# Kernel tuning notes

Hardware: AMD Instinct MI355X
Metric: run time of the kernel (lower is better)

The kernel has to match this reference:

```python
import jax, jax.numpy as jnp
import numpy as np

B, C_MEL, D_RES, TX, TY = 16, 80, 256, 1024, 4096
NEG = -1e9


def seq_mask(lengths, max_len):
    return (jnp.arange(max_len)[None, :] < lengths[:, None]).astype(jnp.float32)


def maximum_path(value, mask):
    # value, mask: [b, tx, ty]. Glow-TTS style monotonic-alignment Viterbi DP.
    b, t_x, t_y = value.shape
    value = value * mask
    x_range = jnp.arange(t_x)[None, :]  # [1, tx]

    def fwd_step(v, inp):
        val_j, j = inp  # val_j: [b, tx]
        v_prev = jnp.pad(v, ((0, 0), (1, 0)), constant_values=NEG)[:, :-1]  # v[x-1]
        stay = v >= v_prev  # True -> best path stays at same x
        v_max = jnp.where(stay, v, v_prev)
        v_new = jnp.where(x_range <= j, v_max + val_j, NEG)
        return v_new, stay

    _, stays = jax.lax.scan(
        fwd_step,
        jnp.zeros((b, t_x), value.dtype),
        (jnp.moveaxis(value, 2, 0), jnp.arange(t_y)),
    )  # stays: [ty, b, tx] bool
    mask_t = jnp.moveaxis(mask, 2, 0)  # [ty, b, tx]
    dirs = jnp.where(mask_t > 0, stays.astype(jnp.int32), 1)  # outside mask: stay

    idx0 = jnp.sum(mask[:, :, 0], axis=1).astype(jnp.int32) - 1  # x_length - 1
    barange = jnp.arange(b)

    def bwd_step(idx, dir_j):  # dir_j: [b, tx]
        row = jax.nn.one_hot(idx, t_x, dtype=value.dtype)  # [b, tx]
        idx_new = idx + dir_j[barange, idx] - 1
        return idx_new, row

    _, path = jax.lax.scan(bwd_step, idx0, dirs, reverse=True)  # [ty, b, tx]
    return jnp.transpose(path, (1, 2, 0)) * mask  # [b, tx, ty]


def setup_inputs() -> dict:
    key = jax.random.key(0)
    k1, k2, k3, k4, k5, k6 = jax.random.split(key, 6)
    return {
        "x_m": jax.random.normal(k1, (B, C_MEL, TX), jnp.float32),
        "x_res": jax.random.normal(k2, (B, D_RES, TX), jnp.float32),
        "mel": jax.random.normal(k3, (B, C_MEL, TY), jnp.float32),
        "x_lengths": jax.random.randint(k4, (B,), TX // 2, TX + 1, jnp.int32),
        "mel_lengths": jax.random.randint(k5, (B,), TY // 2, TY + 1, jnp.int32),
        "noise": jax.random.normal(k6, (B, C_MEL, TY), jnp.float32),
    }


def reference(x_m, x_res, mel, x_lengths, mel_lengths, noise):
    x_mask = seq_mask(x_lengths, TX)[:, None, :]   # [b, 1, tx]
    z_mask = seq_mask(mel_lengths, TY)[:, None, :]  # [b, 1, ty]
    attn_mask = x_mask[:, 0, :, None] * z_mask[:, 0, None, :]  # [b, tx, ty]

    # correlation-style score: -||x_m||^2 - ||mel||^2 + 2 x_m^T mel
    x2 = -jnp.sum(x_m ** 2, axis=1)[:, :, None]   # [b, tx, 1]
    z2 = -jnp.sum(mel ** 2, axis=1)[:, None, :]   # [b, 1, ty]
    xz2 = jnp.einsum("bct,bcs->bts", x_m, mel)    # [b, tx, ty]
    corr = x2 + z2 + 2.0 * xz2

    attn = maximum_path(corr, attn_mask)  # [b, tx, ty], no_grad in original

    z_m = jnp.einsum("bts,bct->bcs", attn, x_res)       # [b, d_res, ty]
    mel_proj = jnp.einsum("bts,bct->bcs", attn, x_m) + noise  # [b, n_mels, ty]
    mel_proj_loss = jnp.mean(jnp.abs((mel_proj - mel) * z_mask))
    logw_ = jnp.log(1e-8 + jnp.sum(attn, axis=-1))[:, None, :] * x_mask  # [b, 1, tx]
    return z_m, z_mask, attn, logw_, mel_proj_loss, mel_proj
```

## Files before the change

### kernel.cpp

```cpp
#include <hip/hip_runtime.h>
#include <cstdint>
#include <cstddef>

typedef unsigned int u32;
typedef unsigned short u16;

#define BB 16
#define CMEL 80
#define DRES 256
#define TXN 1024
#define TYN 4096
#define NEGV (-1e9f)

#define OFF_ZM    0ull
#define OFF_ZMASK 16777216ull
#define OFF_ATTN  16842752ull
#define OFF_LOGW  83951616ull
#define OFF_LOSS  83968000ull
#define OFF_MPROJ 83968001ull

#define WS_X2   0
#define WS_Z2   262144
#define WS_IDX  1310720
#define WS_PART 1572864

__global__ __launch_bounds__(1024) void k1_prep(
    const float* __restrict__ xm, const float* __restrict__ mel,
    const int* __restrict__ mlen,
    float* __restrict__ x2n, float* __restrict__ z2n, float* __restrict__ out_zmask) {
  int b = blockIdx.x;
  int slice = blockIdx.y;
  int t = threadIdx.x;
  if (slice == 0) {
    float acc = 0.f;
    const float* p = xm + (size_t)b * CMEL * TXN + t;
    #pragma unroll 4
    for (int c = 0; c < CMEL; ++c) { float v = p[(size_t)c * TXN]; acc = fmaf(v, v, acc); }
    x2n[b * TXN + t] = -acc;
  } else {
    int j = (slice - 1) * 1024 + t;
    float acc = 0.f;
    const float* p = mel + (size_t)b * CMEL * TYN + j;
    #pragma unroll 4
    for (int c = 0; c < CMEL; ++c) { float v = p[(size_t)c * TYN]; acc = fmaf(v, v, acc); }
    z2n[b * TYN + j] = -acc;
    out_zmask[b * TYN + j] = (j < mlen[b]) ? 1.0f : 0.0f;
  }
}

__global__ __launch_bounds__(256) void k2_corr(
    const float* __restrict__ xm, const float* __restrict__ mel,
    const float* __restrict__ x2n, const float* __restrict__ z2n,
    const int* __restrict__ xlen, const int* __restrict__ mlen,
    float* __restrict__ valT) {
  int b = blockIdx.z;
  int ml = mlen[b];
  int j0 = blockIdx.y * 128;
  if (j0 >= ml) return;
  int xl = xlen[b];
  int x0 = blockIdx.x * 128;

  __shared__ float sA[40][128];
  __shared__ float sB[40][128];

  int t = threadIdx.x;
  int i16 = t & 15, j16 = t >> 4;

  float acc[2][4][2][4];
  #pragma unroll
  for (int p = 0; p < 2; ++p)
    #pragma unroll
    for (int jj = 0; jj < 4; ++jj)
      #pragma unroll
      for (int q = 0; q < 2; ++q)
        #pragma unroll
        for (int i = 0; i < 4; ++i) acc[p][jj][q][i] = 0.f;

  for (int c0 = 0; c0 < CMEL; c0 += 40) {
    __syncthreads();
    for (int i = t; i < 40 * 32; i += 256) {
      int c = i >> 5, q = i & 31;
      *(float4*)&sA[c][q * 4] =
          *(const float4*)(xm + (size_t)(b * CMEL + c0 + c) * TXN + x0 + q * 4);
      *(float4*)&sB[c][q * 4] =
          *(const float4*)(mel + (size_t)(b * CMEL + c0 + c) * TYN + j0 + q * 4);
    }
    __syncthreads();
    #pragma unroll 2
    for (int c = 0; c < 40; ++c) {
      float av[2][4], bw[2][4];
      *(float4*)av[0] = *(const float4*)&sA[c][i16 * 4];
      *(float4*)av[1] = *(const float4*)&sA[c][64 + i16 * 4];
      *(float4*)bw[0] = *(const float4*)&sB[c][j16 * 4];
      *(float4*)bw[1] = *(const float4*)&sB[c][64 + j16 * 4];
      #pragma unroll
      for (int p = 0; p < 2; ++p)
        #pragma unroll
        for (int jj = 0; jj < 4; ++jj)
          #pragma unroll
          for (int q = 0; q < 2; ++q)
            #pragma unroll
            for (int i = 0; i < 4; ++i)
              acc[p][jj][q][i] = fmaf(av[q][i], bw[p][jj], acc[p][jj][q][i]);
    }
  }

  float4 xa[2];
  xa[0] = *(const float4*)(x2n + b * TXN + x0 + i16 * 4);
  xa[1] = *(const float4*)(x2n + b * TXN + x0 + 64 + i16 * 4);
  int xb0 = x0 + i16 * 4;
  int xb1 = x0 + 64 + i16 * 4;

  #pragma unroll
  for (int p = 0; p < 2; ++p)
    #pragma unroll
    for (int jj = 0; jj < 4; ++jj) {
      int j = j0 + p * 64 + j16 * 4 + jj;
      if (j >= ml) continue;
      float zz = z2n[b * TYN + j];
      float* row = valT + ((size_t)b * TYN + j) * TXN;
      float4 o;
      o.x = (xb0 + 0 < xl) ? ((xa[0].x + zz) + 2.f * acc[p][jj][0][0]) : 0.f;
      o.y = (xb0 + 1 < xl) ? ((xa[0].y + zz) + 2.f * acc[p][jj][0][1]) : 0.f;
      o.z = (xb0 + 2 < xl) ? ((xa[0].z + zz) + 2.f * acc[p][jj][0][2]) : 0.f;
      o.w = (xb0 + 3 < xl) ? ((xa[0].w + zz) + 2.f * acc[p][jj][0][3]) : 0.f;
      *(float4*)(row + xb0) = o;
      o.x = (xb1 + 0 < xl) ? ((xa[1].x + zz) + 2.f * acc[p][jj][1][0]) : 0.f;
      o.y = (xb1 + 1 < xl) ? ((xa[1].y + zz) + 2.f * acc[p][jj][1][1]) : 0.f;
      o.z = (xb1 + 2 < xl) ? ((xa[1].z + zz) + 2.f * acc[p][jj][1][2]) : 0.f;
      o.w = (xb1 + 3 < xl) ? ((xa[1].w + zz) + 2.f * acc[p][jj][1][3]) : 0.f;
      *(float4*)(row + xb1) = o;
    }
}

__global__ __launch_bounds__(64) void k3_dp(
    const float* __restrict__ valT, const int* __restrict__ mlen,
    u32* __restrict__ staysW) {
  int b = blockIdx.x;
  int ml = mlen[b];
  int lane = threadIdx.x;
  int xbase = lane << 4;

  float v[16];
  #pragma unroll
  for (int i = 0; i < 16; ++i) v[i] = NEGV;
  if (lane == 0) v[0] = 0.f;

  float4 pf[8][4];
  #pragma unroll
  for (int k = 0; k < 8; ++k) {
    const float* rowp = valT + (((size_t)(b * TYN + k)) << 10);
    #pragma unroll
    for (int q = 0; q < 4; ++q)
      pf[k][q] = *(const float4*)(rowp + (xbase + (q << 2)));
  }

  u32* swb = staysW + (((size_t)(b * TXN + xbase)) << 7);
  int jpad = (ml + 31) & ~31;

  for (int j0 = 0; j0 < jpad; j0 += 32) {
    u32 bits[16];
    #pragma unroll
    for (int i = 0; i < 16; ++i) bits[i] = 0;

    #pragma unroll
    for (int jj = 0; jj < 32; ++jj) {
      const int j = j0 + jj;
      float e = __shfl_up(v[15], 1);
      if (lane == 0) e = NEGV;

      float val[16];
      #pragma unroll
      for (int q = 0; q < 4; ++q) {
        val[4 * q + 0] = pf[jj & 7][q].x;
        val[4 * q + 1] = pf[jj & 7][q].y;
        val[4 * q + 2] = pf[jj & 7][q].z;
        val[4 * q + 3] = pf[jj & 7][q].w;
      }

      #pragma unroll
      for (int i = 15; i >= 1; --i) {
        bool s = v[i] >= v[i - 1];
        float m = s ? v[i] : v[i - 1];
        v[i] = m + val[i];
        bits[i] |= ((u32)s) << jj;
      }
      {
        bool s = v[0] >= e;
        float m = s ? v[0] : e;
        v[0] = m + val[0];
        bits[0] |= ((u32)s) << jj;
      }

      {
        int lt = (j + 1) >> 4;
        if (lane == lt) v[(jj + 1) & 15] = NEGV;
      }

      {
        int jn = j + 8; if (jn > TYN - 1) jn = TYN - 1;
        const float* rowp = valT + (((size_t)(b * TYN + jn)) << 10);
        #pragma unroll
        for (int q = 0; q < 4; ++q)
          pf[jj & 7][q] = *(const float4*)(rowp + (xbase + (q << 2)));
      }
    }

    const int w = j0 >> 5;
    #pragma unroll
    for (int i = 0; i < 16; ++i) swb[(i << 7) + w] = bits[i];
  }
}

__global__ __launch_bounds__(256) void k4_backtrack(
    const u32* __restrict__ staysW, const int* __restrict__ xlen, const int* __restrict__ mlen,
    int* __restrict__ idxArr, float* __restrict__ out_logw) {
  int b = blockIdx.x;
  int xl = xlen[b], ml = mlen[b];
  int t = threadIdx.x;
  __shared__ u32 win[64][128];
  __shared__ u16 lidx[TYN];
  __shared__ u16 ldur[TXN];
  __shared__ int st[3];

  for (int i = t; i < TXN; i += 256) ldur[i] = 0;
  if (t == 0) { st[0] = xl - 1; st[1] = ml - 1; st[2] = ml - 1; }
  __syncthreads();

  int wb = (xl - 1) >> 6;
  for (int i = t; i < 64 * 128; i += 256) {
    int r = i >> 7, wq = i & 127;
    win[r][wq] = staysW[((size_t)(b * TXN + (wb << 6) + r) << 7) + wq];
  }
  __syncthreads();

  while (true) {
    if (t == 0) {
      int idx = st[0], j = st[1], end = st[2];
      while (j >= 0 && (idx >> 6) == wb) {
        u32 w = win[idx & 63][j >> 5];
        int p = j & 31;
        u32 below = w << (31 - p);
        u32 inv = ~below;
        int ones = (inv != 0u) ? __builtin_clz(inv) : 32;
        if (ones > p) {
          j -= p + 1;
        } else {
          int jz = j - ones;
          for (int q = jz; q <= end; ++q) lidx[q] = (u16)idx;
          ldur[idx] = (u16)(end - jz + 1);
          end = jz - 1;
          j = jz - 1;
          idx -= 1;
        }
      }
      if (j < 0) {
        for (int q = 0; q <= end; ++q) lidx[q] = (u16)idx;
        if (idx >= 0 && end >= 0) ldur[idx] = (u16)(end + 1);
      }
      st[0] = idx; st[1] = j; st[2] = end;
    }
    __syncthreads();
    if (st[1] < 0) break;
    wb = st[0] >> 6;
    for (int i = t; i < 64 * 128; i += 256) {
      int r = i >> 7, wq = i & 127;
      win[r][wq] = staysW[((size_t)(b * TXN + (wb << 6) + r) << 7) + wq];
    }
    __syncthreads();
  }

  for (int q = t; q < TYN; q += 256) idxArr[b * TYN + q] = (q < ml) ? (int)lidx[q] : -1;
  for (int x = t; x < TXN; x += 256)
    out_logw[b * TXN + x] = (x < xl) ? logf(1e-8f + (float)ldur[x]) : 0.f;
}

__global__ __launch_bounds__(256) void k5_attn(
    const int* __restrict__ idxArr, float* __restrict__ attn) {
  int b = blockIdx.z;
  int x = blockIdx.y;
  int j = blockIdx.x * 1024 + threadIdx.x * 4;
  int4 iv = *(const int4*)(idxArr + b * TYN + j);
  float4 o;
  o.x = (iv.x == x) ? 1.f : 0.f;
  o.y = (iv.y == x) ? 1.f : 0.f;
  o.z = (iv.z == x) ? 1.f : 0.f;
  o.w = (iv.w == x) ? 1.f : 0.f;
  *(float4*)(attn + ((size_t)(b * TXN + x)) * TYN + j) = o;
}

__global__ __launch_bounds__(256) void k5_zm(
    const int* __restrict__ idxArr, const float* __restrict__ xres, float* __restrict__ zm) {
  int bid = blockIdx.x; int b = bid >> 8; int c = bid & 255;
  const float* row = xres + (size_t)(b * DRES + c) * TXN;
  float* orow = zm + (size_t)(b * DRES + c) * TYN;
  const int* ia = idxArr + b * TYN;
  for (int j = threadIdx.x; j < TYN; j += 256) {
    int idx = ia[j];
    orow[j] = (idx >= 0) ? row[idx] : 0.f;
  }
}

__global__ __launch_bounds__(256) void k5_mproj(
    const int* __restrict__ idxArr, const float* __restrict__ xm,
    const float* __restrict__ noise, const float* __restrict__ mel,
    float* __restrict__ mproj, float* __restrict__ partials) {
  int bid = blockIdx.x; int b = bid / CMEL; int c = bid % CMEL;
  const float* row  = xm    + (size_t)(b * CMEL + c) * TXN;
  const float* nrow = noise + (size_t)(b * CMEL + c) * TYN;
  const float* mrow = mel   + (size_t)(b * CMEL + c) * TYN;
  float* orow = mproj + (size_t)(b * CMEL + c) * TYN;
  const int* ia = idxArr + b * TYN;
  float acc = 0.f;
  for (int j = threadIdx.x; j < TYN; j += 256) {
    int idx = ia[j];
    float g = (idx >= 0) ? row[idx] : 0.f;
    float mp = g + nrow[j];
    orow[j] = mp;
    float d = mp - mrow[j];
    acc += (idx >= 0) ? fabsf(d) : 0.f;
  }
  #pragma unroll
  for (int o = 32; o; o >>= 1) acc += __shfl_down(acc, o);
  __shared__ float ws4[4];
  if ((threadIdx.x & 63) == 0) ws4[threadIdx.x >> 6] = acc;
  __syncthreads();
  if (threadIdx.x == 0) partials[bid] = (ws4[0] + ws4[1]) + (ws4[2] + ws4[3]);
}

__global__ __launch_bounds__(256) void k6_loss(
    const float* __restrict__ partials, float* __restrict__ out_loss) {
  float acc = 0.f;
  for (int i = threadIdx.x; i < BB * CMEL; i += 256) acc += partials[i];
  #pragma unroll
  for (int o = 32; o; o >>= 1) acc += __shfl_down(acc, o);
  __shared__ float ws4[4];
  if ((threadIdx.x & 63) == 0) ws4[threadIdx.x >> 6] = acc;
  __syncthreads();
  if (threadIdx.x == 0)
    out_loss[0] = ((ws4[0] + ws4[1]) + (ws4[2] + ws4[3])) * (1.0f / ((float)BB * CMEL * TYN));
}

extern "C" void kernel_launch(void* const* d_in, const int* in_sizes, int n_in,
                              void* d_out, int out_size, void* d_ws, size_t ws_size,
                              hipStream_t stream) {
  const float* xm    = (const float*)d_in[0];
  const float* xres  = (const float*)d_in[1];
  const float* mel   = (const float*)d_in[2];
  const int*   xlen  = (const int*)d_in[3];
  const int*   mlen  = (const int*)d_in[4];
  const float* noise = (const float*)d_in[5];

  float* out = (float*)d_out;
  float* out_zm    = out + OFF_ZM;
  float* out_zmask = out + OFF_ZMASK;
  float* out_attn  = out + OFF_ATTN;
  float* out_logw  = out + OFF_LOGW;
  float* out_loss  = out + OFF_LOSS;
  float* out_mproj = out + OFF_MPROJ;

  char* ws = (char*)d_ws;
  float* x2n      = (float*)(ws + WS_X2);
  float* z2n      = (float*)(ws + WS_Z2);
  int*   idxArr   = (int*)(ws + WS_IDX);
  float* partials = (float*)(ws + WS_PART);

  float* valT   = out_attn;
  u32*   staysW = (u32*)out_zm;

  hipLaunchKernelGGL(k1_prep, dim3(BB, 5), dim3(1024), 0, stream, xm, mel, mlen, x2n, z2n, out_zmask);
  hipLaunchKernelGGL(k2_corr, dim3(8, 32, BB), dim3(256), 0, stream, xm, mel, x2n, z2n, xlen, mlen, valT);
  hipLaunchKernelGGL(k3_dp, dim3(BB), dim3(64), 0, stream, valT, mlen, staysW);
  hipLaunchKernelGGL(k4_backtrack, dim3(BB), dim3(256), 0, stream, staysW, xlen, mlen, idxArr, out_logw);
  hipLaunchKernelGGL(k5_attn, dim3(4, TXN, BB), dim3(256), 0, stream, idxArr, out_attn);
  hipLaunchKernelGGL(k5_zm, dim3(BB * DRES), dim3(256), 0, stream, idxArr, xres, out_zm);
  hipLaunchKernelGGL(k5_mproj, dim3(BB * CMEL), dim3(256), 0, stream, idxArr, xm, noise, mel, out_mproj, partials);
  hipLaunchKernelGGL(k6_loss, dim3(1), dim3(256), 0, stream, partials, out_loss);
}
```

Measured before the change: 1.202 ms.

## Stream DP value rows through LDS ring buffer with async global-to-LDS loads

The serial Viterbi DP kernel now prefetches value rows with global_load_lds into a 12-row LDS ring buffer, replacing the 8-deep register prefetch. A manual vmcnt wait keeps about 11 rows in flight, and a small register double-buffer reads from LDS two steps ahead. The bit-packing of stay flags changes from 32-bit words per 32 steps to 16-bit halves per 16 steps, which pads the tail less, and the select is replaced by fmaxf. The aim is to hide global memory latency on the single-wave latency-bound recurrence, at the cost of hand-tuned waitcnt counts and a different stays word layout that the backtrack must still read correctly.

```diff
diff --git a/kernel.cpp b/kernel.cpp
--- a/kernel.cpp
+++ b/kernel.cpp
@@ -23,6 +23,10 @@
 #define WS_Z2   262144
 #define WS_IDX  1310720
 #define WS_PART 1572864
+
+#define GLLDS(gp, lp) \
+  __builtin_amdgcn_global_load_lds((const __attribute__((address_space(1))) void*)(gp), \
+                                   (__attribute__((address_space(3))) void*)(lp), 16, 0, 0)
 
 __global__ __launch_bounds__(1024) void k1_prep(
     const float* __restrict__ xm, const float* __restrict__ mel,
@@ -133,82 +137,107 @@
     }
 }
 
+#define NR 12
 __global__ __launch_bounds__(64) void k3_dp(
     const float* __restrict__ valT, const int* __restrict__ mlen,
     u32* __restrict__ staysW) {
-  int b = blockIdx.x;
-  int ml = mlen[b];
-  int lane = threadIdx.x;
-  int xbase = lane << 4;
+  __shared__ float lds[NR * 1024];
+  const int b = blockIdx.x;
+  const int ml = mlen[b];
+  const int lane = threadIdx.x;
+  const float* vb = valT + ((size_t)b << 22);
+
+  for (int r = 0; r < NR - 1; ++r) {
+    const float* gp = vb + ((size_t)r << 10) + (lane << 4);
+    float* lp = &lds[r << 10];
+    GLLDS(gp,      lp);
+    GLLDS(gp + 4,  lp + 256);
+    GLLDS(gp + 8,  lp + 512);
+    GLLDS(gp + 12, lp + 768);
+  }
 
   float v[16];
   #pragma unroll
   for (int i = 0; i < 16; ++i) v[i] = NEGV;
   if (lane == 0) v[0] = 0.f;
 
-  float4 pf[8][4];
-  #pragma unroll
-  for (int k = 0; k < 8; ++k) {
-    const float* rowp = valT + (((size_t)(b * TYN + k)) << 10);
+  asm volatile("s_waitcnt vmcnt(36)" ::: "memory");
+  float4 vbuf[4][4];
+  #pragma unroll
+  for (int q = 0; q < 4; ++q) {
+    vbuf[0][q] = *(const float4*)&lds[(0 << 10) + (q << 8) + (lane << 2)];
+    vbuf[1][q] = *(const float4*)&lds[(1 << 10) + (q << 8) + (lane << 2)];
+  }
+
+  int wSlot = NR - 1;
+  int rSlot = 2;
+  int gRow  = NR - 1;
+
+  u16* sw16 = (u16*)staysW + (((size_t)(b * TXN + (lane << 4))) << 8);
+
+  const int jpad = (ml + 15) & ~15;
+  for (int j0 = 0; j0 < jpad; j0 += 16) {
+    u32 bh[16];
     #pragma unroll
-    for (int q = 0; q < 4; ++q)
-      pf[k][q] = *(const float4*)(rowp + (xbase + (q << 2)));
-  }
-
-  u32* swb = staysW + (((size_t)(b * TXN + xbase)) << 7);
-  int jpad = (ml + 31) & ~31;
-
-  for (int j0 = 0; j0 < jpad; j0 += 32) {
-    u32 bits[16];
+    for (int i = 0; i < 16; ++i) bh[i] = 0;
+
     #pragma unroll
-    for (int i = 0; i < 16; ++i) bits[i] = 0;
-
+    for (int jj = 0; jj < 16; ++jj) {
+      const int j = j0 + jj;
+
+      {
+        const float* gp = vb + ((size_t)gRow << 10) + (lane << 4);
+        float* lp = &lds[wSlot << 10];
+        GLLDS(gp,      lp);
+        GLLDS(gp + 4,  lp + 256);
+        GLLDS(gp + 8,  lp + 512);
+        GLLDS(gp + 12, lp + 768);
+        wSlot = (wSlot == NR - 1) ? 0 : wSlot + 1;
+        gRow += (gRow < TYN - 1) ? 1 : 0;
+      }
+
+      asm volatile("s_waitcnt vmcnt(36)" ::: "memory");
+
+      {
+        float e = __shfl_up(v[15], 1);
+        if (lane == 0) e = NEGV;
+
+        float val[16];
+        #pragma unroll
+        for (int q = 0; q < 4; ++q) {
+          val[4 * q + 0] = vbuf[jj & 3][q].x;
+          val[4 * q + 1] = vbuf[jj & 3][q].y;
+          val[4 * q + 2] = vbuf[jj & 3][q].z;
+          val[4 * q + 3] = vbuf[jj & 3][q].w;
+        }
+
+        #pragma unroll
+        for (int i = 15; i >= 1; --i) {
+          bool s = v[i] >= v[i - 1];
+          v[i] = fmaxf(v[i], v[i - 1]) + val[i];
+          bh[i] |= ((u32)s) << jj;
+        }
+        {
+          bool s = v[0] >= e;
+          v[0] = fmaxf(v[0], e) + val[0];
+          bh[0] |= ((u32)s) << jj;
+        }
+
+        {
+          int lt = (j + 1) >> 4;
+          if (lane == lt) v[(jj + 1) & 15] = NEGV;
+        }
+      }
+
+      #pragma unroll
+      for (int q = 0; q < 4; ++q)
+        vbuf[(jj + 2) & 3][q] = *(const float4*)&lds[(rSlot << 10) + (q << 8) + (lane << 2)];
+      rSlot = (rSlot == NR - 1) ? 0 : rSlot + 1;
+    }
+
+    const int h = j0 >> 4;
     #pragma unroll
-    for (int jj = 0; jj < 32; ++jj) {
-      const int j = j0 + jj;
-      float e = __shfl_up(v[15], 1);
-      if (lane == 0) e = NEGV;
-
-      float val[16];
-      #pragma unroll
-      for (int q = 0; q < 4; ++q) {
-        val[4 * q + 0] = pf[jj & 7][q].x;
-        val[4 * q + 1] = pf[jj & 7][q].y;
-        val[4 * q + 2] = pf[jj & 7][q].z;
-        val[4 * q + 3] = pf[jj & 7][q].w;
-      }
-
-      #pragma unroll
-      for (int i = 15; i >= 1; --i) {
-        bool s = v[i] >= v[i - 1];
-        float m = s ? v[i] : v[i - 1];
-        v[i] = m + val[i];
-        bits[i] |= ((u32)s) << jj;
-      }
-      {
-        bool s = v[0] >= e;
-        float m = s ? v[0] : e;
-        v[0] = m + val[0];
-        bits[0] |= ((u32)s) << jj;
-      }
-
-      {
-        int lt = (j + 1) >> 4;
-        if (lane == lt) v[(jj + 1) & 15] = NEGV;
-      }
-
-      {
-        int jn = j + 8; if (jn > TYN - 1) jn = TYN - 1;
-        const float* rowp = valT + (((size_t)(b * TYN + jn)) << 10);
-        #pragma unroll
-        for (int q = 0; q < 4; ++q)
-          pf[jj & 7][q] = *(const float4*)(rowp + (xbase + (q << 2)));
-      }
-    }
-
-    const int w = j0 >> 5;
-    #pragma unroll
-    for (int i = 0; i < 16; ++i) swb[(i << 7) + w] = bits[i];
+    for (int i = 0; i < 16; ++i) sw16[(i << 8) + h] = (u16)bh[i];
   }
 }
 
```

Result: slower. 2.072 ms (+72.3%).
